# Kernel optimization log

Measured on AMD Instinct MI355X. Metric: run time of the kernel, lower is better.

## Reference

```python
import jax, jax.numpy as jnp
import numpy as np

B, S, V = 256, 8, 32000
PLACEHOLDER = -1


def setup_inputs() -> dict:
    key = jax.random.key(0)
    ks = jax.random.split(key, 8)
    rng = np.random.default_rng(0)
    lens = rng.integers(1, S + 1, size=B)          # ragged draft lengths per request
    cu = np.cumsum(lens).astype(np.int32)
    N = int(cu[-1])
    draft_token_ids = jax.random.randint(ks[0], (N,), 0, V, dtype=jnp.int32)
    dp = jax.random.uniform(ks[1], (N, V), dtype=jnp.float32)
    draft_probs = dp / dp.sum(-1, keepdims=True)
    tp = jax.random.uniform(ks[2], (N, V), dtype=jnp.float32)
    target_probs = tp / tp.sum(-1, keepdims=True)
    bonus_token_ids = jax.random.randint(ks[3], (B,), 0, V, dtype=jnp.int32)
    uniform_probs = jax.random.uniform(ks[4], (N,), dtype=jnp.float32)
    is_greedy = jax.random.uniform(ks[5], (B,)) < 0.5
    q = jax.random.exponential(ks[6], (B, V), dtype=jnp.float32)  # Gumbel-trick noise
    return dict(draft_probs=draft_probs, target_probs=target_probs,
                uniform_probs=uniform_probs, q=q,
                cu_num_draft_tokens=jnp.asarray(cu), draft_token_ids=draft_token_ids,
                bonus_token_ids=bonus_token_ids, is_greedy=is_greedy, max_spec_len=S)


def reference(draft_probs, target_probs, uniform_probs, q,
              cu_num_draft_tokens, draft_token_ids, bonus_token_ids,
              is_greedy, max_spec_len):
    cu = cu_num_draft_tokens
    b = cu.shape[0]
    n = draft_token_ids.shape[0]
    s = int(max_spec_len)
    starts = jnp.concatenate([jnp.zeros((1,), cu.dtype), cu[:-1]])
    lens = cu - starts                                   # [B]
    tok_idx = jnp.arange(n)
    tok_req = jnp.searchsorted(cu, tok_idx, side='right')  # [N] request id per token
    pos = tok_idx - starts[tok_req]                        # [N] position within request

    # greedy branch: accept while draft matches target argmax, emit target argmax
    target_argmax = jnp.argmax(target_probs, axis=-1).astype(jnp.int32)  # [N]

    # random branch: accept iff draft_prob>0 and target/draft >= u
    d_at = draft_probs[tok_idx, draft_token_ids]
    t_at = target_probs[tok_idx, draft_token_ids]
    rnd_accept = (d_at > 0) & (t_at >= uniform_probs * d_at)

    # recovered tokens: argmax over vocab of max(target-draft,0)/q (exp-noise sampling)
    recovered = jnp.argmax(jnp.maximum(target_probs - draft_probs, 0.0) / q[tok_req],
                           axis=-1).astype(jnp.int32)     # [N]

    greedy_t = is_greedy[tok_req]
    accept = jnp.where(greedy_t, draft_token_ids == target_argmax, rnd_accept)
    token = jnp.where(greedy_t, target_argmax,
                      jnp.where(rnd_accept, draft_token_ids, recovered))

    # densify ragged tokens to [B, S]; padding positions count as accepted
    dense_acc = jnp.ones((b, s), bool).at[tok_req, pos].set(accept)
    dense_val = jnp.zeros((b, s), bool).at[tok_req, pos].set(True)
    dense_tok = jnp.full((b, s), PLACEHOLDER, jnp.int32).at[tok_req, pos].set(token)

    # early-exit scan: position p is written iff all positions < p were accepted
    cm = jnp.cumprod(dense_acc.astype(jnp.int32), axis=1).astype(bool)
    excl = jnp.concatenate([jnp.ones((b, 1), bool), cm[:, :-1]], axis=1)
    write = excl & dense_val
    body = jnp.where(write, dense_tok, PLACEHOLDER)
    out = jnp.concatenate([body, jnp.full((b, 1), PLACEHOLDER, jnp.int32)], axis=1)

    # bonus token if every draft token was accepted
    rows = jnp.arange(b)
    out = out.at[rows, lens].set(jnp.where(cm[:, -1], bonus_token_ids, out[rows, lens]))
    return out
```

## Files before the change

### kernel.cpp

```cpp
#include <hip/hip_runtime.h>

#define PLACEHOLDER (-1)
#define T  1024
#define NW (T / 64)

__device__ __forceinline__ void comb(float& v, int& i, float v2, int i2) {
    if (v2 > v || (v2 == v && i2 < i)) { v = v2; i = i2; }
}

__device__ __forceinline__ void block_argmax(float& bv, int& bi, float* s_v, int* s_i) {
    #pragma unroll
    for (int off = 32; off > 0; off >>= 1) {
        float v2 = __shfl_down(bv, off);
        int   i2 = __shfl_down(bi, off);
        comb(bv, bi, v2, i2);
    }
    const int tid = threadIdx.x;
    if ((tid & 63) == 0) { s_v[tid >> 6] = bv; s_i[tid >> 6] = bi; }
    __syncthreads();
    float rv = s_v[0]; int ri = s_i[0];
    #pragma unroll
    for (int w = 1; w < NW; ++w) comb(rv, ri, s_v[w], s_i[w]);
    bv = rv; bi = ri;
}

#define PROC_T(t, base)                                   \
    do {                                                  \
        if ((t).x > bv) { bv = (t).x; bi = (base);     }  \
        if ((t).y > bv) { bv = (t).y; bi = (base) + 1; }  \
        if ((t).z > bv) { bv = (t).z; bi = (base) + 2; }  \
        if ((t).w > bv) { bv = (t).w; bi = (base) + 3; }  \
    } while (0)

#define PROC_R(t, d, qq, base)                                                  \
    do {                                                                        \
        float r_;                                                               \
        r_ = fmaxf((t).x - (d).x, 0.0f) / (qq).x; if (r_ > bv) { bv = r_; bi = (base);     } \
        r_ = fmaxf((t).y - (d).y, 0.0f) / (qq).y; if (r_ > bv) { bv = r_; bi = (base) + 1; } \
        r_ = fmaxf((t).z - (d).z, 0.0f) / (qq).z; if (r_ > bv) { bv = r_; bi = (base) + 2; } \
        r_ = fmaxf((t).w - (d).w, 0.0f) / (qq).w; if (r_ > bv) { bv = r_; bi = (base) + 3; } \
    } while (0)

__global__ __launch_bounds__(T) void fused_one(
    const float* __restrict__ dp, const float* __restrict__ tp,
    const float* __restrict__ up, const float* __restrict__ q,
    const int* __restrict__ cu, const int* __restrict__ did,
    const int* __restrict__ bonus, const void* __restrict__ grd,
    int* __restrict__ out, int B, int V, int S)
{
    const int b = blockIdx.x, tid = threadIdx.x;
    __shared__ float s_v[NW];
    __shared__ int   s_i[NW];
    __shared__ int   sh_g, sh_fr;

    const int start = b ? cu[b - 1] : 0;
    const int len   = cu[b] - start;
    const int V4    = V >> 2;
    int* row = out + b * (S + 1);

    if (tid < 64) {
        bool f0 = false, f1 = false;
        for (int t = tid; t * 4 < B; t += 64) {
            const unsigned w = ((const unsigned*)grd)[t];
            if (w & 0xFEFEFEFEu) f0 = true;
            if (w & 0x01010100u) f1 = true;
        }
        const bool enc_f32  = (__ballot(f0) != 0ull);
        const bool enc_byte = !enc_f32 && (__ballot(f1) != 0ull);
        const bool g = enc_f32  ? (((const float*)grd)[b] != 0.0f)
                     : enc_byte ? (((const unsigned char*)grd)[b] != 0)
                                : (((const int*)grd)[b] != 0);
        int fr = len;
        if (!g) {
            bool acc = true;
            if (tid < len) {
                const int i  = start + tid;
                const int td = did[i];
                const float dat = dp[(size_t)i * V + td];
                const float tat = tp[(size_t)i * V + td];
                acc = (dat > 0.0f && tat >= up[i] * dat);
            }
            const unsigned long long rej =
                (~__ballot(acc)) & ((len >= 64) ? ~0ull : ((1ull << len) - 1ull));
            fr = rej ? (__ffsll((long long)rej) - 1) : len;
        }
        if (tid == 0) { sh_g = g ? 1 : 0; sh_fr = fr; }
    }
    __syncthreads();
    const bool g  = (sh_g != 0);
    const int  fr = sh_fr;

    int scan_row = -1, kind = 0;
    if (g)            { scan_row = start;      kind = 1; }
    else if (fr < len){ scan_row = start + fr; kind = 0; }

    float bv = 0.0f; int bi = 0x7FFFFFFF;
    if (scan_row >= 0) {
        if (kind) {
            const float4* t4 = (const float4*)(tp + (size_t)scan_row * V);
            int j = tid;
            for (; j + T < V4; j += 2 * T) {
                const float4 ta = t4[j];
                const float4 tb = t4[j + T];
                PROC_T(ta, j << 2);
                PROC_T(tb, (j + T) << 2);
            }
            for (; j < V4; j += T) { const float4 t = t4[j]; PROC_T(t, j << 2); }
            for (int j2 = (V4 << 2) + tid; j2 < V; j2 += T) {
                const float tv = tp[(size_t)scan_row * V + j2];
                if (tv > bv) { bv = tv; bi = j2; }
            }
        } else {
            const float4* t4 = (const float4*)(tp + (size_t)scan_row * V);
            const float4* d4 = (const float4*)(dp + (size_t)scan_row * V);
            const float4* q4 = (const float4*)(q  + (size_t)b * V);
            int j = tid;
            for (; j + T < V4; j += 2 * T) {
                const float4 ta = t4[j],     da = d4[j],     qa = q4[j];
                const float4 tb = t4[j + T], db = d4[j + T], qb = q4[j + T];
                PROC_R(ta, da, qa, j << 2);
                PROC_R(tb, db, qb, (j + T) << 2);
            }
            for (; j < V4; j += T) {
                const float4 t = t4[j], d = d4[j], qq = q4[j];
                PROC_R(t, d, qq, j << 2);
            }
            for (int j2 = (V4 << 2) + tid; j2 < V; j2 += T) {
                const float r = fmaxf(tp[(size_t)scan_row * V + j2]
                                      - dp[(size_t)scan_row * V + j2], 0.0f)
                                / q[(size_t)b * V + j2];
                if (r > bv) { bv = r; bi = j2; }
            }
        }
        block_argmax(bv, bi, s_v, s_i);
    }

    if (!g) {
        if (tid <= S) {
            int val;
            if (tid < fr)       val = did[start + tid];
            else if (fr < len)  val = (tid == fr)  ? bi       : PLACEHOLDER;
            else                val = (tid == len) ? bonus[b] : PLACEHOLDER;
            row[tid] = val;
        }
        return;
    }

    const int tok0 = bi;
    const bool ok0 = (did[start] == tok0);
    if (!ok0 || len == 1) {
        if (tid <= S) {
            int val = PLACEHOLDER;
            if (tid == 0) val = tok0;
            else if (ok0 && tid == len) val = bonus[b];
            row[tid] = val;
        }
        return;
    }
    if (tid == 0) row[0] = tok0;
    bool ok = true;
    int p = 1;
    for (; p < len && ok; ++p) {
        __syncthreads();
        const float4* t4 = (const float4*)(tp + (size_t)(start + p) * V);
        float cv = 0.0f; int ci = 0x7FFFFFFF;
        for (int j = tid; j < V4; j += T) {
            const float4 t = t4[j]; const int base = j << 2;
            if (t.x > cv) { cv = t.x; ci = base;     }
            if (t.y > cv) { cv = t.y; ci = base + 1; }
            if (t.z > cv) { cv = t.z; ci = base + 2; }
            if (t.w > cv) { cv = t.w; ci = base + 3; }
        }
        for (int j = (V4 << 2) + tid; j < V; j += T) {
            const float tv = tp[(size_t)(start + p) * V + j];
            if (tv > cv) { cv = tv; ci = j; }
        }
        block_argmax(cv, ci, s_v, s_i);
        if (tid == 0) row[p] = ci;
        ok = (did[start + p] == ci);
    }
    if (tid == 0) {
        for (int r = p; r <= S; ++r) row[r] = PLACEHOLDER;
        if (ok) row[len] = bonus[b];
    }
}

extern "C" void kernel_launch(void* const* d_in, const int* in_sizes, int n_in,
                              void* d_out, int out_size, void* d_ws, size_t ws_size,
                              hipStream_t stream) {
    const float* dp  = (const float*)d_in[0];
    const float* tp  = (const float*)d_in[1];
    const float* up  = (const float*)d_in[2];
    const float* q   = (const float*)d_in[3];
    const int*   cu  = (const int*)d_in[4];
    const int*   did = (const int*)d_in[5];
    const int*   bon = (const int*)d_in[6];
    const void*  grd = d_in[7];

    const int B = in_sizes[4];
    const int N = in_sizes[5];
    const int V = in_sizes[0] / N;
    const int S = out_size / B - 1;

    fused_one<<<B, T, 0, stream>>>(dp, tp, up, q, cu, did, bon, grd,
                                   (int*)d_out, B, V, S);
}
```

Baseline: 17.50 us.

## Split each request's vocab scan across eight blocks with spin-wait cross-block merge

```diff
diff --git a/kernel.cpp b/kernel.cpp
--- a/kernel.cpp
+++ b/kernel.cpp
@@ -1,7 +1,8 @@
 #include <hip/hip_runtime.h>
 
 #define PLACEHOLDER (-1)
-#define T  1024
+#define KB 8
+#define T  256
 #define NW (T / 64)
 
 __device__ __forceinline__ void comb(float& v, int& i, float v2, int i2) {
@@ -41,17 +42,25 @@
         r_ = fmaxf((t).w - (d).w, 0.0f) / (qq).w; if (r_ > bv) { bv = r_; bi = (base) + 3; } \
     } while (0)
 
-__global__ __launch_bounds__(T) void fused_one(
+__device__ __forceinline__ unsigned long long pack_vi(float v, int i) {
+    return ((unsigned long long)__float_as_uint(v) << 32)
+         | (unsigned long long)(0xFFFFFFFFu - (unsigned)i);
+}
+
+__global__ __launch_bounds__(T) void fused_spread(
     const float* __restrict__ dp, const float* __restrict__ tp,
     const float* __restrict__ up, const float* __restrict__ q,
     const int* __restrict__ cu, const int* __restrict__ did,
     const int* __restrict__ bonus, const void* __restrict__ grd,
-    int* __restrict__ out, int B, int V, int S)
+    int* __restrict__ out, unsigned long long* __restrict__ slots,
+    unsigned long long* __restrict__ shadow, int B, int V, int S)
 {
-    const int b = blockIdx.x, tid = threadIdx.x;
+    const int blk = blockIdx.x;
+    const int b = blk >> 3, slice = blk & (KB - 1);
+    const int tid = threadIdx.x;
     __shared__ float s_v[NW];
     __shared__ int   s_i[NW];
-    __shared__ int   sh_g, sh_fr;
+    __shared__ int   sh_g, sh_fr, sh_bi;
 
     const int start = b ? cu[b - 1] : 0;
     const int len   = cu[b] - start;
@@ -91,48 +100,67 @@
     const int  fr = sh_fr;
 
     int scan_row = -1, kind = 0;
-    if (g)            { scan_row = start;      kind = 1; }
-    else if (fr < len){ scan_row = start + fr; kind = 0; }
+    if (g)             { scan_row = start;      kind = 1; }
+    else if (fr < len) { scan_row = start + fr; kind = 0; }
 
     float bv = 0.0f; int bi = 0x7FFFFFFF;
     if (scan_row >= 0) {
+        const int c4 = (V4 + KB - 1) / KB;
+        const int j0 = slice * c4;
+        const int j1 = min(j0 + c4, V4);
         if (kind) {
             const float4* t4 = (const float4*)(tp + (size_t)scan_row * V);
-            int j = tid;
-            for (; j + T < V4; j += 2 * T) {
-                const float4 ta = t4[j];
-                const float4 tb = t4[j + T];
-                PROC_T(ta, j << 2);
-                PROC_T(tb, (j + T) << 2);
-            }
-            for (; j < V4; j += T) { const float4 t = t4[j]; PROC_T(t, j << 2); }
-            for (int j2 = (V4 << 2) + tid; j2 < V; j2 += T) {
-                const float tv = tp[(size_t)scan_row * V + j2];
-                if (tv > bv) { bv = tv; bi = j2; }
-            }
+            for (int j = j0 + tid; j < j1; j += T) {
+                const float4 t = t4[j];
+                PROC_T(t, j << 2);
+            }
+            if (slice == KB - 1)
+                for (int j2 = (V4 << 2) + tid; j2 < V; j2 += T) {
+                    const float tv = tp[(size_t)scan_row * V + j2];
+                    if (tv > bv) { bv = tv; bi = j2; }
+                }
         } else {
             const float4* t4 = (const float4*)(tp + (size_t)scan_row * V);
             const float4* d4 = (const float4*)(dp + (size_t)scan_row * V);
             const float4* q4 = (const float4*)(q  + (size_t)b * V);
-            int j = tid;
-            for (; j + T < V4; j += 2 * T) {
-                const float4 ta = t4[j],     da = d4[j],     qa = q4[j];
-                const float4 tb = t4[j + T], db = d4[j + T], qb = q4[j + T];
-                PROC_R(ta, da, qa, j << 2);
-                PROC_R(tb, db, qb, (j + T) << 2);
-            }
-            for (; j < V4; j += T) {
+            for (int j = j0 + tid; j < j1; j += T) {
                 const float4 t = t4[j], d = d4[j], qq = q4[j];
                 PROC_R(t, d, qq, j << 2);
             }
-            for (int j2 = (V4 << 2) + tid; j2 < V; j2 += T) {
-                const float r = fmaxf(tp[(size_t)scan_row * V + j2]
-                                      - dp[(size_t)scan_row * V + j2], 0.0f)
-                                / q[(size_t)b * V + j2];
-                if (r > bv) { bv = r; bi = j2; }
-            }
+            if (slice == KB - 1)
+                for (int j2 = (V4 << 2) + tid; j2 < V; j2 += T) {
+                    const float r = fmaxf(tp[(size_t)scan_row * V + j2]
+                                          - dp[(size_t)scan_row * V + j2], 0.0f)
+                                    / q[(size_t)b * V + j2];
+                    if (r > bv) { bv = r; bi = j2; }
+                }
         }
         block_argmax(bv, bi, s_v, s_i);
+
+        if (slice != 0) {
+            if (tid == 0) {
+                const unsigned long long pk = pack_vi(bv, bi);
+                atomicExch(&slots[blk], pk);
+                atomicExch(&shadow[blk], ~pk);
+            }
+            return;
+        }
+        if (tid == 0) {
+            for (int s = 1; s < KB; ++s) {
+                unsigned long long pk, sh;
+                do {
+                    pk = atomicAdd(&slots[(b << 3) + s], 0ull);
+                    sh = atomicAdd(&shadow[(b << 3) + s], 0ull);
+                } while (pk == 0ull || (pk >> 63) || sh != ~pk);
+                comb(bv, bi, __uint_as_float((unsigned)(pk >> 32)),
+                     (int)(0xFFFFFFFFu - (unsigned)pk));
+            }
+            sh_bi = bi;
+        }
+        __syncthreads();
+        bi = sh_bi;
+    } else if (slice != 0) {
+        return;
     }
 
     if (!g) {
@@ -202,6 +230,9 @@
     const int V = in_sizes[0] / N;
     const int S = out_size / B - 1;
 
-    fused_one<<<B, T, 0, stream>>>(dp, tp, up, q, cu, did, bon, grd,
-                                   (int*)d_out, B, V, S);
-}
+    unsigned long long* slots  = (unsigned long long*)d_ws;
+    unsigned long long* shadow = slots + (size_t)B * KB;
+
+    fused_spread<<<B * KB, T, 0, stream>>>(dp, tp, up, q, cu, did, bon, grd,
+                                           (int*)d_out, slots, shadow, B, V, S);
+}
```

After: 18.82 us. 1.08x slower.
